# Kernel tuning notes

Hardware: AMD Instinct MI355X
Metric: run time of the kernel (lower is better)

The kernel has to match this reference:

```python
import jax, jax.numpy as jnp
import numpy as np

N_TREES = 512
DEPTH = 10
NODES_PER_TREE = 2 ** DEPTH - 1  # 1023, heap-indexed complete binary tree
N = N_TREES * NODES_PER_TREE     # 523776 nodes
X_SIZE = 128
H_SIZE = 128
NUM_CLASSES = 5
VOCAB = 32000


def _level_ids(l):
    """Global node ids for level l (root=0) and their child ids (None for leaves)."""
    start = 2 ** l - 1
    heap = start + np.arange(2 ** l)
    tree_off = np.arange(N_TREES)[:, None] * NODES_PER_TREE
    ids = (tree_off + heap[None, :]).reshape(-1)
    if l < DEPTH - 1:
        child_heap = np.stack([2 * heap + 1, 2 * heap + 2], axis=-1)  # [2^l, 2]
        child = (np.arange(N_TREES)[:, None, None] * NODES_PER_TREE
                 + child_heap[None]).reshape(-1, 2)
        return jnp.asarray(ids), jnp.asarray(child)
    return jnp.asarray(ids), None


def setup_inputs() -> dict:
    key = jax.random.key(0)
    ks = jax.random.split(key, 12)
    s = 0.05
    return {
        "wordid": jax.random.randint(ks[0], (N,), 0, VOCAB),
        "E":      jax.random.normal(ks[1], (VOCAB, X_SIZE), jnp.float32) * s,
        "W_iou":  jax.random.normal(ks[2], (3 * H_SIZE, X_SIZE), jnp.float32) * s,
        "b_iou":  jax.random.normal(ks[3], (3 * H_SIZE,), jnp.float32) * s,
        "U_iou":  jax.random.normal(ks[4], (3 * H_SIZE, H_SIZE), jnp.float32) * s,
        "b_Uiou": jax.random.normal(ks[5], (3 * H_SIZE,), jnp.float32) * s,
        "W_f":    jax.random.normal(ks[6], (H_SIZE, X_SIZE), jnp.float32) * s,
        "b_Wf":   jax.random.normal(ks[7], (H_SIZE,), jnp.float32) * s,
        "U_f":    jax.random.normal(ks[8], (H_SIZE, H_SIZE), jnp.float32) * s,
        "b_Uf":   jax.random.normal(ks[9], (H_SIZE,), jnp.float32) * s,
        "W_out":  jax.random.normal(ks[10], (NUM_CLASSES, H_SIZE), jnp.float32) * s,
        "b_out":  jax.random.normal(ks[11], (NUM_CLASSES,), jnp.float32) * s,
    }


def reference(wordid, E, W_iou, b_iou, U_iou, b_Uiou, W_f, b_Wf, U_f, b_Uf, W_out, b_out):
    mask = (wordid != -1)  # PAD_WORD mask; all-true for generated ids
    x = E[wordid * mask.astype(wordid.dtype)] * mask[:, None].astype(E.dtype)  # [N, X]

    h = jnp.zeros((N, H_SIZE), E.dtype)
    c = jnp.zeros((N, H_SIZE), E.dtype)

    # Topological traversal: leaves (deepest level) up to roots.
    for l in reversed(range(DEPTH)):
        ids, child = _level_ids(l)
        xl = x[ids]  # [M, X]
        if child is None:  # leaves: empty mailbox -> h_tild = c_tild = 0
            h_tild = jnp.zeros((ids.shape[0], H_SIZE), E.dtype)
            c_tild = h_tild
        else:
            hc = h[child]                               # mailbox h: [M, 2, H]
            cc = c[child]                               # mailbox c: [M, 2, H]
            h_tild = hc.sum(axis=1)                     # child-sum
            wx = xl @ W_f.T + b_Wf                      # [M, H]
            uh = hc @ U_f.T + b_Uf                      # [M, 2, H]
            f = jax.nn.sigmoid(wx[:, None, :] + uh)     # per-child forget gate
            c_tild = (f * cc).sum(axis=1)
        iou = xl @ W_iou.T + b_iou + h_tild @ U_iou.T + b_Uiou  # [M, 3H]
        i, o, u = jnp.split(iou, 3, axis=1)
        i, o, u = jax.nn.sigmoid(i), jax.nn.sigmoid(o), jnp.tanh(u)
        cl = i * u + c_tild
        hl = o * jnp.tanh(cl)
        h = h.at[ids].set(hl)
        c = c.at[ids].set(cl)

    # dropout is identity in eval / p=0.0
    logits = h @ W_out.T + b_out  # [N, num_classes]
    return logits
```

## Files before the change

kernel.cpp:

```cpp
#include <hip/hip_runtime.h>

#define H 128
#define TDEPTH 10
#define NPT 1023
#define NTREES 512

typedef unsigned short bf16_t;
typedef unsigned int u32;
typedef __attribute__((ext_vector_type(8))) short bf16x8;
typedef __attribute__((ext_vector_type(4))) float f32x4;

__device__ __forceinline__ float rcp_(float x) { return __builtin_amdgcn_rcpf(x); }
__device__ __forceinline__ float sig_(float x) { return rcp_(1.0f + __expf(-x)); }
__device__ __forceinline__ float th_(float x)  { return 1.0f - 2.0f * rcp_(__expf(2.0f * x) + 1.0f); }
__device__ __forceinline__ float b2f(u32 u) {
    union { float f; u32 u; } v; v.u = u << 16; return v.f;
}
__device__ __forceinline__ bf16_t f2b16(float f) {
    union { float f; u32 u; } v; v.f = f;
    return (bf16_t)((v.u + 0x7fffu + ((v.u >> 16) & 1u)) >> 16);
}
__device__ __forceinline__ bf16x8 ld8(const bf16_t* p) {
    return *reinterpret_cast<const bf16x8*>(p);
}
__device__ __forceinline__ bf16x8 ld8c(const char* p) {
    return *reinterpret_cast<const bf16x8*>(p);
}
__device__ __forceinline__ void gload16(const void* g, void* l) {
    __builtin_amdgcn_global_load_lds(
        (const __attribute__((address_space(1))) void*)g,
        (__attribute__((address_space(3))) void*)l, 16, 0, 0);
}
#define MFMA(a,b,c) __builtin_amdgcn_mfma_f32_16x16x32_bf16(a,b,c,0,0,0)

#define R_H  8192
#define R_C  24576
#define BUFSZ 40960

__global__ void pack_weights(const float* __restrict__ W_iou, const float* __restrict__ U_iou,
                             const float* __restrict__ W_f,   const float* __restrict__ U_f,
                             const float* __restrict__ W_out, bf16_t* __restrict__ Wb)
{
    int i = blockIdx.x * 256 + threadIdx.x;
    if (i < 131072) {
        int k    = i & 127;
        int p    = (i >> 7) & 7;
        int feat = i >> 10;
        float v;
        switch (p) {
            case 0: v = W_iou[(      feat) * H + k]; break;
            case 1: v = W_iou[(128 + feat) * H + k]; break;
            case 2: v = W_iou[(256 + feat) * H + k]; break;
            case 3: v = U_iou[(      feat) * H + k]; break;
            case 4: v = U_iou[(128 + feat) * H + k]; break;
            case 5: v = U_iou[(256 + feat) * H + k]; break;
            case 6: v = W_f  [feat * H + k]; break;
            default: v = U_f [feat * H + k]; break;
        }
        Wb[i] = f2b16(v);
    } else {
        int j = i - 131072;
        int cls = j >> 7, k = j & 127;
        Wb[i] = f2b16(cls < 5 ? W_out[cls * H + k] : 0.0f);
    }
}

__global__ void pack_E(const float* __restrict__ E, bf16_t* __restrict__ Eb)
{
    int i = blockIdx.x * 256 + threadIdx.x;
    Eb[i] = f2b16(E[i]);
}

__global__ __launch_bounds__(512, 4) void leaf_mfma(
    const int* __restrict__ wordid, const bf16_t* __restrict__ Eb,
    const bf16_t* __restrict__ Wb,
    const float* __restrict__ b_iou, const float* __restrict__ b_Uiou,
    bf16_t* __restrict__ h_cur, bf16_t* __restrict__ c_cur, int t0)
{
    const int level = TDEPTH - 1;
    __shared__ __align__(16) char x_s[64 * 256];

    const int tid = threadIdx.x;
    const int n0  = blockIdx.x * 64;

    for (int idx = tid; idx < 1024; idx += 512) {
        int q = idx & 15, m = idx >> 4;
        int g = n0 + m;
        int t = g >> level, i = g & ((1 << level) - 1);
        int wid = wordid[(t0 + t) * NPT + (1 << level) - 1 + i];
        *(uint4*)(x_s + m * 256 + ((q * 16) ^ ((m & 7) << 4))) =
            *(const uint4*)(Eb + (size_t)wid * H + q * 8);
    }
    __syncthreads();

    const int lane = tid & 63;
    const int w    = tid >> 6;
    const int l15  = lane & 15;
    const int kg   = lane >> 4;
    const int feat = w * 16 + l15;
    const bf16_t* wbase = Wb + (size_t)feat * 1024 + kg * 8;

    f32x4 z = {0.f, 0.f, 0.f, 0.f};
    f32x4 acc[3][4];
#pragma unroll
    for (int g = 0; g < 3; ++g)
#pragma unroll
        for (int m = 0; m < 4; ++m) acc[g][m] = z;

#pragma unroll
    for (int ks = 0; ks < 4; ++ks) {
        bf16x8 W0 = ld8(wbase + ks * 32 + 0 * 128);
        bf16x8 W1 = ld8(wbase + ks * 32 + 1 * 128);
        bf16x8 W2 = ld8(wbase + ks * 32 + 2 * 128);
        const int cb = (ks * 32 + kg * 8) * 2;
#pragma unroll
        for (int mt = 0; mt < 4; ++mt) {
            int row = mt * 16 + l15;
            bf16x8 xa = ld8c(x_s + row * 256 + (cb ^ ((row & 7) << 4)));
            acc[0][mt] = MFMA(xa, W0, acc[0][mt]);
            acc[1][mt] = MFMA(xa, W1, acc[1][mt]);
            acc[2][mt] = MFMA(xa, W2, acc[2][mt]);
        }
    }

    float bi = b_iou[      feat] + b_Uiou[      feat];
    float bo = b_iou[128 + feat] + b_Uiou[128 + feat];
    float bu = b_iou[256 + feat] + b_Uiou[256 + feat];
#pragma unroll
    for (int mt = 0; mt < 4; ++mt) {
#pragma unroll
        for (int r = 0; r < 4; ++r) {
            int g = n0 + mt * 16 + kg * 4 + r;
            float iv = sig_(acc[0][mt][r] + bi);
            float ov = sig_(acc[1][mt][r] + bo);
            float uv = th_ (acc[2][mt][r] + bu);
            float cl = iv * uv;
            float hl = ov * th_(cl);
            h_cur[(size_t)g * H + feat] = f2b16(hl);
            c_cur[(size_t)g * H + feat] = f2b16(cl);
        }
    }
}

__global__ __launch_bounds__(512, 2) void internal_mfma(
    const int* __restrict__ wordid, const bf16_t* __restrict__ Eb,
    const bf16_t* __restrict__ Wb,
    const float* __restrict__ b_iou, const float* __restrict__ b_Uiou,
    const float* __restrict__ b_Wf,  const float* __restrict__ b_Uf,
    const bf16_t* __restrict__ h_prev, const bf16_t* __restrict__ c_prev,
    bf16_t* __restrict__ h_cur, bf16_t* __restrict__ c_cur,
    const float* __restrict__ b_out, float* __restrict__ out,
    int level, int t0, int nt)
{
    extern __shared__ __align__(16) char lds_raw[];

    const int tid  = threadIdx.x;
    const int lane = tid & 63;
    const int w    = tid >> 6;
    const int l15  = lane & 15;
    const int kg   = lane >> 4;
    const int feat = w * 16 + l15;
    const int tilebase = blockIdx.x * nt;

    const float bi  = b_iou[      feat] + b_Uiou[      feat];
    const float bo  = b_iou[128 + feat] + b_Uiou[128 + feat];
    const float bu  = b_iou[256 + feat] + b_Uiou[256 + feat];
    const float bfv = b_Wf[feat] + b_Uf[feat];
    const bf16_t* wbase = Wb + (size_t)feat * 1024 + kg * 8;
    const f32x4 z = {0.f, 0.f, 0.f, 0.f};

    const int lrow = lane >> 4;
    const int colb = (lane & 15) * 16;

    auto issue = [&](int t, char* buf) {
        int n0 = (tilebase + t) * 32;
#pragma unroll
        for (int cc = 0; cc < 5; ++cc) {
            int ch = w + cc * 8;
            const char* src;
            if (ch < 8) {
                int row = ch * 4 + lrow;
                int g = n0 + row;
                int tt = g >> level, ii = g & ((1 << level) - 1);
                int wid = wordid[(t0 + tt) * NPT + (1 << level) - 1 + ii];
                src = (const char*)Eb + (size_t)wid * 256 + (colb ^ ((row & 7) << 4));
            } else if (ch < 24) {
                int row = (ch - 8) * 4 + lrow;
                src = (const char*)h_prev + ((size_t)(2 * n0) + row) * 256
                    + (colb ^ (((row >> 1) & 7) << 4));
            } else {
                int row = (ch - 24) * 4 + lrow;
                src = (const char*)c_prev + ((size_t)(2 * n0) + row) * 256
                    + (colb ^ ((row & 7) << 4));
            }
            gload16(src, buf + ch * 1024);
        }
    };

    issue(0, lds_raw);
    __syncthreads();

    for (int t = 0; t < nt; ++t) {
        char* buf = lds_raw + (t & 1) * BUFSZ;
        char* x_s = buf;
        char* h_s = buf + R_H;
        char* c_s = buf + R_C;
        const int n0 = (tilebase + t) * 32;

        f32x4 acc[6][2];
#pragma unroll
        for (int g = 0; g < 6; ++g)
#pragma unroll
            for (int m = 0; m < 2; ++m) acc[g][m] = z;

#pragma unroll
        for (int ks = 0; ks < 4; ++ks) {
            bf16x8 W0 = ld8(wbase + ks * 32 + 0 * 128);
            bf16x8 W1 = ld8(wbase + ks * 32 + 1 * 128);
            bf16x8 W2 = ld8(wbase + ks * 32 + 2 * 128);
            bf16x8 W3 = ld8(wbase + ks * 32 + 3 * 128);
            bf16x8 W4 = ld8(wbase + ks * 32 + 4 * 128);
            bf16x8 W5 = ld8(wbase + ks * 32 + 5 * 128);
            bf16x8 W6 = ld8(wbase + ks * 32 + 6 * 128);
            bf16x8 W7 = ld8(wbase + ks * 32 + 7 * 128);
            const int cb = (ks * 32 + kg * 8) * 2;
#pragma unroll
            for (int mt = 0; mt < 2; ++mt) {
                const int row = mt * 16 + l15;
                const int sw  = (row & 7) << 4;
                bf16x8 xa  = ld8c(x_s + row * 256 + (cb ^ sw));
                bf16x8 h0a = ld8c(h_s + (2 * row)     * 256 + (cb ^ sw));
                bf16x8 h1a = ld8c(h_s + (2 * row + 1) * 256 + (cb ^ sw));
                acc[0][mt] = MFMA(h1a, W3, MFMA(h0a, W3, MFMA(xa, W0, acc[0][mt])));
                acc[1][mt] = MFMA(h1a, W4, MFMA(h0a, W4, MFMA(xa, W1, acc[1][mt])));
                acc[2][mt] = MFMA(h1a, W5, MFMA(h0a, W5, MFMA(xa, W2, acc[2][mt])));
                acc[3][mt] = MFMA(xa,  W6, acc[3][mt]);
                acc[4][mt] = MFMA(h0a, W7, acc[4][mt]);
                acc[5][mt] = MFMA(h1a, W7, acc[5][mt]);
            }
        }

        if (w < 4) {
            const int pr = (w & 2) ? 1 : 0;
            const int mbase = (w & 1) * 16;
            const bf16_t* Wob = Wb + 131072;
            f32x4 lacc = z;
#pragma unroll
            for (int ks = 0; ks < 4; ++ks) {
                const int cb = (ks * 32 + kg * 8) * 2;
                int prow = mbase + l15;
                bf16x8 ha = ld8c(h_s + (size_t)(2 * prow + pr) * 256
                                 + (cb ^ ((prow & 7) << 4)));
                bf16x8 wo = ld8(Wob + (size_t)l15 * 128 + ks * 32 + kg * 8);
                lacc = MFMA(ha, wo, lacc);
            }
            if (l15 < 5) {
                float bo5 = b_out[l15];
                int lc = level + 1;
#pragma unroll
                for (int r = 0; r < 4; ++r) {
                    int m  = mbase + kg * 4 + r;
                    int gc = 2 * (n0 + m) + pr;
                    int tt = gc >> lc, ii = gc & ((1 << lc) - 1);
                    out[(size_t)((t0 + tt) * NPT + (1 << lc) - 1 + ii) * 5 + l15] = lacc[r] + bo5;
                }
            }
        }

        if (t + 1 < nt) issue(t + 1, lds_raw + ((t + 1) & 1) * BUFSZ);

#pragma unroll
        for (int mt = 0; mt < 2; ++mt) {
#pragma unroll
            for (int r = 0; r < 4; ++r) {
                int nb = mt * 16 + kg * 4 + r;
                int g  = n0 + nb;
                float iv = sig_(acc[0][mt][r] + bi);
                float ov = sig_(acc[1][mt][r] + bo);
                float uv = th_ (acc[2][mt][r] + bu);
                float fx = acc[3][mt][r];
                float f0 = sig_(fx + acc[4][mt][r] + bfv);
                float f1 = sig_(fx + acc[5][mt][r] + bfv);
                float c0 = b2f((u32)*(const bf16_t*)(c_s + (2 * nb) * 256
                              + ((feat * 2) ^ (((2 * nb) & 7) << 4))));
                float c1 = b2f((u32)*(const bf16_t*)(c_s + (2 * nb + 1) * 256
                              + ((feat * 2) ^ (((2 * nb + 1) & 7) << 4))));
                float cl = iv * uv + f0 * c0 + f1 * c1;
                float hl = ov * th_(cl);
                h_cur[(size_t)g * H + feat] = f2b16(hl);
                c_cur[(size_t)g * H + feat] = f2b16(cl);
            }
        }

        __syncthreads();
    }
}

__global__ void logits_root(
    const bf16_t* __restrict__ h0buf, const float* __restrict__ W_out,
    const float* __restrict__ b_out, float* __restrict__ out,
    int M, int t0)
{
    int wv     = (blockIdx.x * blockDim.x + threadIdx.x) >> 6;
    int lane   = threadIdx.x & 63;
    int nwaves = (gridDim.x * blockDim.x) >> 6;
    for (int g = wv; g < M; g += nwaves) {
        float h0 = b2f((u32)h0buf[(size_t)g * H + lane]);
        float h1 = b2f((u32)h0buf[(size_t)g * H + 64 + lane]);
#pragma unroll
        for (int c = 0; c < 5; ++c) {
            float p = h0 * W_out[c * H + lane] + h1 * W_out[c * H + 64 + lane];
#pragma unroll
            for (int off = 32; off >= 1; off >>= 1) p += __shfl_xor(p, off, 64);
            if (lane == 0) out[(size_t)(t0 + g) * NPT * 5 + c] = p + b_out[c];
        }
    }
}

extern "C" void kernel_launch(void* const* d_in, const int* in_sizes, int n_in,
                              void* d_out, int out_size, void* d_ws, size_t ws_size,
                              hipStream_t stream)
{
    (void)in_sizes; (void)n_in; (void)out_size;
    const int*   wordid = (const int*)  d_in[0];
    const float* E      = (const float*)d_in[1];
    const float* W_iou  = (const float*)d_in[2];
    const float* b_iou  = (const float*)d_in[3];
    const float* U_iou  = (const float*)d_in[4];
    const float* b_Uiou = (const float*)d_in[5];
    const float* W_f    = (const float*)d_in[6];
    const float* b_Wf   = (const float*)d_in[7];
    const float* U_f    = (const float*)d_in[8];
    const float* b_Uf   = (const float*)d_in[9];
    const float* W_out  = (const float*)d_in[10];
    const float* b_out  = (const float*)d_in[11];
    float* out = (float*)d_out;

    bf16_t* Wb = (bf16_t*)d_ws;
    bf16_t* Eb = Wb + 133120;
    bf16_t* dyn = Eb + (size_t)32000 * H;
    const size_t fixed_bytes = (133120 + (size_t)32000 * H) * 2;

    int C = 1;
    while (C < 16 && fixed_bytes + (size_t)(NTREES / C) * 393216u > ws_size) C <<= 1;
    const int T = NTREES / C;

    bf16_t* hA = dyn;
    bf16_t* cA = hA + (size_t)T * 512 * H;
    bf16_t* hB = cA + (size_t)T * 512 * H;
    bf16_t* cB = hB + (size_t)T * 256 * H;

    pack_weights<<<520, 256, 0, stream>>>(W_iou, U_iou, W_f, U_f, W_out, Wb);
    pack_E<<<16000, 256, 0, stream>>>(E, Eb);

    for (int chunk = 0; chunk < C; ++chunk) {
        int t0 = chunk * T;
        for (int l = TDEPTH - 1; l >= 0; --l) {
            int M = T << l;
            bf16_t* h_cur  = (l & 1) ? hA : hB;
            bf16_t* c_cur  = (l & 1) ? cA : cB;
            bf16_t* h_prev = (l & 1) ? hB : hA;
            bf16_t* c_prev = (l & 1) ? cB : cA;

            if (l == TDEPTH - 1) {
                leaf_mfma<<<M / 64, 512, 0, stream>>>(
                    wordid, Eb, Wb, b_iou, b_Uiou, h_cur, c_cur, t0);
            } else {
                int tiles  = M / 32;
                int blocks = tiles < 512 ? tiles : 512;
                int nt     = tiles / blocks;
                internal_mfma<<<blocks, 512, 2 * BUFSZ, stream>>>(
                    wordid, Eb, Wb, b_iou, b_Uiou, b_Wf, b_Uf,
                    h_prev, c_prev, h_cur, c_cur, b_out, out, l, t0, nt);
            }
        }
        int blocksR = (T / 4 < 4096) ? ((T + 3) / 4) : 4096;
        if (blocksR < 1) blocksR = 1;
        logits_root<<<blocksR, 256, 0, stream>>>(hB, W_out, b_out, out, T, t0);
    }
}
```

Baseline: 388.1 us.

## Hoist weight fragments into registers, issue prefetch earlier, halve internal grid

```diff
diff --git a/kernel.cpp b/kernel.cpp
--- a/kernel.cpp
+++ b/kernel.cpp
@@ -166,8 +166,20 @@
     const float bo  = b_iou[128 + feat] + b_Uiou[128 + feat];
     const float bu  = b_iou[256 + feat] + b_Uiou[256 + feat];
     const float bfv = b_Wf[feat] + b_Uf[feat];
+    const f32x4 z = {0.f, 0.f, 0.f, 0.f};
+
     const bf16_t* wbase = Wb + (size_t)feat * 1024 + kg * 8;
-    const f32x4 z = {0.f, 0.f, 0.f, 0.f};
+    const bf16_t* Wob   = Wb + 131072;
+    bf16x8 Wr[4][8];
+#pragma unroll
+    for (int ks = 0; ks < 4; ++ks)
+#pragma unroll
+        for (int p = 0; p < 8; ++p)
+            Wr[ks][p] = ld8(wbase + ks * 32 + p * 128);
+    bf16x8 Lr[4];
+#pragma unroll
+    for (int ks = 0; ks < 4; ++ks)
+        Lr[ks] = ld8(Wob + (size_t)l15 * 128 + ks * 32 + kg * 8);
 
     const int lrow = lane >> 4;
     const int colb = (lane & 15) * 16;
@@ -215,14 +227,6 @@
 
 #pragma unroll
         for (int ks = 0; ks < 4; ++ks) {
-            bf16x8 W0 = ld8(wbase + ks * 32 + 0 * 128);
-            bf16x8 W1 = ld8(wbase + ks * 32 + 1 * 128);
-            bf16x8 W2 = ld8(wbase + ks * 32 + 2 * 128);
-            bf16x8 W3 = ld8(wbase + ks * 32 + 3 * 128);
-            bf16x8 W4 = ld8(wbase + ks * 32 + 4 * 128);
-            bf16x8 W5 = ld8(wbase + ks * 32 + 5 * 128);
-            bf16x8 W6 = ld8(wbase + ks * 32 + 6 * 128);
-            bf16x8 W7 = ld8(wbase + ks * 32 + 7 * 128);
             const int cb = (ks * 32 + kg * 8) * 2;
 #pragma unroll
             for (int mt = 0; mt < 2; ++mt) {
@@ -231,19 +235,20 @@
                 bf16x8 xa  = ld8c(x_s + row * 256 + (cb ^ sw));
                 bf16x8 h0a = ld8c(h_s + (2 * row)     * 256 + (cb ^ sw));
                 bf16x8 h1a = ld8c(h_s + (2 * row + 1) * 256 + (cb ^ sw));
-                acc[0][mt] = MFMA(h1a, W3, MFMA(h0a, W3, MFMA(xa, W0, acc[0][mt])));
-                acc[1][mt] = MFMA(h1a, W4, MFMA(h0a, W4, MFMA(xa, W1, acc[1][mt])));
-                acc[2][mt] = MFMA(h1a, W5, MFMA(h0a, W5, MFMA(xa, W2, acc[2][mt])));
-                acc[3][mt] = MFMA(xa,  W6, acc[3][mt]);
-                acc[4][mt] = MFMA(h0a, W7, acc[4][mt]);
-                acc[5][mt] = MFMA(h1a, W7, acc[5][mt]);
-            }
-        }
+                acc[0][mt] = MFMA(h1a, Wr[ks][3], MFMA(h0a, Wr[ks][3], MFMA(xa, Wr[ks][0], acc[0][mt])));
+                acc[1][mt] = MFMA(h1a, Wr[ks][4], MFMA(h0a, Wr[ks][4], MFMA(xa, Wr[ks][1], acc[1][mt])));
+                acc[2][mt] = MFMA(h1a, Wr[ks][5], MFMA(h0a, Wr[ks][5], MFMA(xa, Wr[ks][2], acc[2][mt])));
+                acc[3][mt] = MFMA(xa,  Wr[ks][6], acc[3][mt]);
+                acc[4][mt] = MFMA(h0a, Wr[ks][7], acc[4][mt]);
+                acc[5][mt] = MFMA(h1a, Wr[ks][7], acc[5][mt]);
+            }
+        }
+
+        if (t + 1 < nt) issue(t + 1, lds_raw + ((t + 1) & 1) * BUFSZ);
 
         if (w < 4) {
             const int pr = (w & 2) ? 1 : 0;
             const int mbase = (w & 1) * 16;
-            const bf16_t* Wob = Wb + 131072;
             f32x4 lacc = z;
 #pragma unroll
             for (int ks = 0; ks < 4; ++ks) {
@@ -251,8 +256,7 @@
                 int prow = mbase + l15;
                 bf16x8 ha = ld8c(h_s + (size_t)(2 * prow + pr) * 256
                                  + (cb ^ ((prow & 7) << 4)));
-                bf16x8 wo = ld8(Wob + (size_t)l15 * 128 + ks * 32 + kg * 8);
-                lacc = MFMA(ha, wo, lacc);
+                lacc = MFMA(ha, Lr[ks], lacc);
             }
             if (l15 < 5) {
                 float bo5 = b_out[l15];
@@ -266,8 +270,6 @@
                 }
             }
         }
-
-        if (t + 1 < nt) issue(t + 1, lds_raw + ((t + 1) & 1) * BUFSZ);
 
 #pragma unroll
         for (int mt = 0; mt < 2; ++mt) {
@@ -367,7 +369,7 @@
                     wordid, Eb, Wb, b_iou, b_Uiou, h_cur, c_cur, t0);
             } else {
                 int tiles  = M / 32;
-                int blocks = tiles < 512 ? tiles : 512;
+                int blocks = tiles < 256 ? tiles : 256;
                 int nt     = tiles / blocks;
                 internal_mfma<<<blocks, 512, 2 * BUFSZ, stream>>>(
                     wordid, Eb, Wb, b_iou, b_Uiou, b_Wf, b_Uf,
```

Result: no change. 392.7 us (+1.2%).

## Halve internal tile to 16 nodes, prefetch word ids, issue next tile earlier

Applied to the files above, without the earlier changes.

```diff
diff --git a/kernel.cpp b/kernel.cpp
--- a/kernel.cpp
+++ b/kernel.cpp
@@ -33,9 +33,9 @@
 }
 #define MFMA(a,b,c) __builtin_amdgcn_mfma_f32_16x16x32_bf16(a,b,c,0,0,0)
 
-#define R_H  8192
-#define R_C  24576
-#define BUFSZ 40960
+#define R_H  4096
+#define R_C  12288
+#define BUFSZ 20480
 
 __global__ void pack_weights(const float* __restrict__ W_iou, const float* __restrict__ U_iou,
                              const float* __restrict__ W_f,   const float* __restrict__ U_f,
@@ -142,7 +142,7 @@
     }
 }
 
-__global__ __launch_bounds__(512, 2) void internal_mfma(
+__global__ __launch_bounds__(512, 4) void internal_mfma(
     const int* __restrict__ wordid, const bf16_t* __restrict__ Eb,
     const bf16_t* __restrict__ Wb,
     const float* __restrict__ b_iou, const float* __restrict__ b_Uiou,
@@ -166,38 +166,48 @@
     const float bo  = b_iou[128 + feat] + b_Uiou[128 + feat];
     const float bu  = b_iou[256 + feat] + b_Uiou[256 + feat];
     const float bfv = b_Wf[feat] + b_Uf[feat];
+    const f32x4 z = {0.f, 0.f, 0.f, 0.f};
+
     const bf16_t* wbase = Wb + (size_t)feat * 1024 + kg * 8;
-    const f32x4 z = {0.f, 0.f, 0.f, 0.f};
+    const bf16_t* Wob   = Wb + 131072;
 
     const int lrow = lane >> 4;
     const int colb = (lane & 15) * 16;
 
-    auto issue = [&](int t, char* buf) {
-        int n0 = (tilebase + t) * 32;
-#pragma unroll
-        for (int cc = 0; cc < 5; ++cc) {
+    auto loadwid = [&](int n0x) -> int {
+        int row = w * 4 + lrow;
+        int g = n0x + row;
+        int tt = g >> level, ii = g & ((1 << level) - 1);
+        return wordid[(t0 + tt) * NPT + (1 << level) - 1 + ii];
+    };
+
+    auto issue = [&](int n0x, int widv, char* buf) {
+#pragma unroll
+        for (int cc = 0; cc < 3; ++cc) {
             int ch = w + cc * 8;
-            const char* src;
-            if (ch < 8) {
-                int row = ch * 4 + lrow;
-                int g = n0 + row;
-                int tt = g >> level, ii = g & ((1 << level) - 1);
-                int wid = wordid[(t0 + tt) * NPT + (1 << level) - 1 + ii];
-                src = (const char*)Eb + (size_t)wid * 256 + (colb ^ ((row & 7) << 4));
-            } else if (ch < 24) {
-                int row = (ch - 8) * 4 + lrow;
-                src = (const char*)h_prev + ((size_t)(2 * n0) + row) * 256
-                    + (colb ^ (((row >> 1) & 7) << 4));
-            } else {
-                int row = (ch - 24) * 4 + lrow;
-                src = (const char*)c_prev + ((size_t)(2 * n0) + row) * 256
-                    + (colb ^ ((row & 7) << 4));
+            if (ch < 20) {
+                const char* src;
+                if (ch < 4) {
+                    int row = ch * 4 + lrow;
+                    src = (const char*)Eb + (size_t)widv * 256 + (colb ^ ((row & 7) << 4));
+                } else if (ch < 12) {
+                    int j = (ch - 4) * 4 + lrow;
+                    src = (const char*)h_prev + ((size_t)(2 * n0x) + j) * 256
+                        + (colb ^ (((j >> 1) & 7) << 4));
+                } else {
+                    int j = (ch - 12) * 4 + lrow;
+                    src = (const char*)c_prev + ((size_t)(2 * n0x) + j) * 256
+                        + (colb ^ ((j & 7) << 4));
+                }
+                gload16(src, buf + ch * 1024);
             }
-            gload16(src, buf + ch * 1024);
         }
     };
 
-    issue(0, lds_raw);
+    int widcur = 0;
+    if (w < 4) widcur = loadwid(tilebase * 16);
+    issue(tilebase * 16, widcur, lds_raw);
+    if (nt > 1 && w < 4) widcur = loadwid((tilebase + 1) * 16);
     __syncthreads();
 
     for (int t = 0; t < nt; ++t) {
@@ -205,13 +215,16 @@
         char* x_s = buf;
         char* h_s = buf + R_H;
         char* c_s = buf + R_C;
-        const int n0 = (tilebase + t) * 32;
-
-        f32x4 acc[6][2];
-#pragma unroll
-        for (int g = 0; g < 6; ++g)
-#pragma unroll
-            for (int m = 0; m < 2; ++m) acc[g][m] = z;
+        const int n0 = (tilebase + t) * 16;
+
+        if (t + 1 < nt)
+            issue((tilebase + t + 1) * 16, widcur, lds_raw + ((t + 1) & 1) * BUFSZ);
+        int widnext = widcur;
+        if (t + 2 < nt && w < 4) widnext = loadwid((tilebase + t + 2) * 16);
+
+        f32x4 acc[6];
+#pragma unroll
+        for (int g = 0; g < 6; ++g) acc[g] = z;
 
 #pragma unroll
         for (int ks = 0; ks < 4; ++ks) {
@@ -224,33 +237,26 @@
             bf16x8 W6 = ld8(wbase + ks * 32 + 6 * 128);
             bf16x8 W7 = ld8(wbase + ks * 32 + 7 * 128);
             const int cb = (ks * 32 + kg * 8) * 2;
-#pragma unroll
-            for (int mt = 0; mt < 2; ++mt) {
-                const int row = mt * 16 + l15;
-                const int sw  = (row & 7) << 4;
-                bf16x8 xa  = ld8c(x_s + row * 256 + (cb ^ sw));
-                bf16x8 h0a = ld8c(h_s + (2 * row)     * 256 + (cb ^ sw));
-                bf16x8 h1a = ld8c(h_s + (2 * row + 1) * 256 + (cb ^ sw));
-                acc[0][mt] = MFMA(h1a, W3, MFMA(h0a, W3, MFMA(xa, W0, acc[0][mt])));
-                acc[1][mt] = MFMA(h1a, W4, MFMA(h0a, W4, MFMA(xa, W1, acc[1][mt])));
-                acc[2][mt] = MFMA(h1a, W5, MFMA(h0a, W5, MFMA(xa, W2, acc[2][mt])));
-                acc[3][mt] = MFMA(xa,  W6, acc[3][mt]);
-                acc[4][mt] = MFMA(h0a, W7, acc[4][mt]);
-                acc[5][mt] = MFMA(h1a, W7, acc[5][mt]);
-            }
-        }
-
-        if (w < 4) {
-            const int pr = (w & 2) ? 1 : 0;
-            const int mbase = (w & 1) * 16;
-            const bf16_t* Wob = Wb + 131072;
+            const int sw = (l15 & 7) << 4;
+            bf16x8 xa  = ld8c(x_s + l15 * 256 + (cb ^ sw));
+            bf16x8 h0a = ld8c(h_s + (2 * l15)     * 256 + (cb ^ sw));
+            bf16x8 h1a = ld8c(h_s + (2 * l15 + 1) * 256 + (cb ^ sw));
+            acc[0] = MFMA(h1a, W3, MFMA(h0a, W3, MFMA(xa, W0, acc[0])));
+            acc[1] = MFMA(h1a, W4, MFMA(h0a, W4, MFMA(xa, W1, acc[1])));
+            acc[2] = MFMA(h1a, W5, MFMA(h0a, W5, MFMA(xa, W2, acc[2])));
+            acc[3] = MFMA(xa,  W6, acc[3]);
+            acc[4] = MFMA(h0a, W7, acc[4]);
+            acc[5] = MFMA(h1a, W7, acc[5]);
+        }
+
+        if (w < 2) {
+            const int pr = w;
             f32x4 lacc = z;
 #pragma unroll
             for (int ks = 0; ks < 4; ++ks) {
                 const int cb = (ks * 32 + kg * 8) * 2;
-                int prow = mbase + l15;
-                bf16x8 ha = ld8c(h_s + (size_t)(2 * prow + pr) * 256
-                                 + (cb ^ ((prow & 7) << 4)));
+                bf16x8 ha = ld8c(h_s + (size_t)(2 * l15 + pr) * 256
+                                 + (cb ^ ((l15 & 7) << 4)));
                 bf16x8 wo = ld8(Wob + (size_t)l15 * 128 + ks * 32 + kg * 8);
                 lacc = MFMA(ha, wo, lacc);
             }
@@ -259,7 +265,7 @@
                 int lc = level + 1;
 #pragma unroll
                 for (int r = 0; r < 4; ++r) {
-                    int m  = mbase + kg * 4 + r;
+                    int m  = kg * 4 + r;
                     int gc = 2 * (n0 + m) + pr;
                     int tt = gc >> lc, ii = gc & ((1 << lc) - 1);
                     out[(size_t)((t0 + tt) * NPT + (1 << lc) - 1 + ii) * 5 + l15] = lacc[r] + bo5;
@@ -267,31 +273,27 @@
             }
         }
 
-        if (t + 1 < nt) issue(t + 1, lds_raw + ((t + 1) & 1) * BUFSZ);
-
-#pragma unroll
-        for (int mt = 0; mt < 2; ++mt) {
-#pragma unroll
-            for (int r = 0; r < 4; ++r) {
-                int nb = mt * 16 + kg * 4 + r;
-                int g  = n0 + nb;
-                float iv = sig_(acc[0][mt][r] + bi);
-                float ov = sig_(acc[1][mt][r] + bo);
-                float uv = th_ (acc[2][mt][r] + bu);
-                float fx = acc[3][mt][r];
-                float f0 = sig_(fx + acc[4][mt][r] + bfv);
-                float f1 = sig_(fx + acc[5][mt][r] + bfv);
-                float c0 = b2f((u32)*(const bf16_t*)(c_s + (2 * nb) * 256
-                              + ((feat * 2) ^ (((2 * nb) & 7) << 4))));
-                float c1 = b2f((u32)*(const bf16_t*)(c_s + (2 * nb + 1) * 256
-                              + ((feat * 2) ^ (((2 * nb + 1) & 7) << 4))));
-                float cl = iv * uv + f0 * c0 + f1 * c1;
-                float hl = ov * th_(cl);
-                h_cur[(size_t)g * H + feat] = f2b16(hl);
-                c_cur[(size_t)g * H + feat] = f2b16(cl);
-            }
-        }
-
+#pragma unroll
+        for (int r = 0; r < 4; ++r) {
+            int nb = kg * 4 + r;
+            int g  = n0 + nb;
+            float iv = sig_(acc[0][r] + bi);
+            float ov = sig_(acc[1][r] + bo);
+            float uv = th_ (acc[2][r] + bu);
+            float fx = acc[3][r];
+            float f0 = sig_(fx + acc[4][r] + bfv);
+            float f1 = sig_(fx + acc[5][r] + bfv);
+            float c0 = b2f((u32)*(const bf16_t*)(c_s + (2 * nb) * 256
+                          + ((feat * 2) ^ (((2 * nb) & 7) << 4))));
+            float c1 = b2f((u32)*(const bf16_t*)(c_s + (2 * nb + 1) * 256
+                          + ((feat * 2) ^ (((2 * nb + 1) & 7) << 4))));
+            float cl = iv * uv + f0 * c0 + f1 * c1;
+            float hl = ov * th_(cl);
+            h_cur[(size_t)g * H + feat] = f2b16(hl);
+            c_cur[(size_t)g * H + feat] = f2b16(cl);
+        }
+
+        widcur = widnext;
         __syncthreads();
     }
 }
@@ -366,7 +368,7 @@
                 leaf_mfma<<<M / 64, 512, 0, stream>>>(
                     wordid, Eb, Wb, b_iou, b_Uiou, h_cur, c_cur, t0);
             } else {
-                int tiles  = M / 32;
+                int tiles  = M / 16;
                 int blocks = tiles < 512 ? tiles : 512;
                 int nt     = tiles / blocks;
                 internal_mfma<<<blocks, 512, 2 * BUFSZ, stream>>>(
```

Measured after the change: 708.0 us. 82.5% more time.

## Fuse leaf level and its parent level into one kernel via LDS

Applied to the files above, without the earlier changes.

```diff
diff --git a/kernel.cpp b/kernel.cpp
--- a/kernel.cpp
+++ b/kernel.cpp
@@ -36,6 +36,11 @@
 #define R_H  8192
 #define R_C  24576
 #define BUFSZ 40960
+
+#define FX_SZ   24576
+#define F_H     49152
+#define F_C     65536
+#define F_LDSSZ 81920
 
 __global__ void pack_weights(const float* __restrict__ W_iou, const float* __restrict__ U_iou,
                              const float* __restrict__ W_f,   const float* __restrict__ U_f,
@@ -71,74 +76,204 @@
     Eb[i] = f2b16(E[i]);
 }
 
-__global__ __launch_bounds__(512, 4) void leaf_mfma(
+__global__ __launch_bounds__(512, 2) void leaf8_fused(
     const int* __restrict__ wordid, const bf16_t* __restrict__ Eb,
     const bf16_t* __restrict__ Wb,
     const float* __restrict__ b_iou, const float* __restrict__ b_Uiou,
-    bf16_t* __restrict__ h_cur, bf16_t* __restrict__ c_cur, int t0)
+    const float* __restrict__ b_Wf,  const float* __restrict__ b_Uf,
+    bf16_t* __restrict__ h_cur, bf16_t* __restrict__ c_cur,
+    const float* __restrict__ b_out, float* __restrict__ out,
+    int t0, int nt)
 {
-    const int level = TDEPTH - 1;
-    __shared__ __align__(16) char x_s[64 * 256];
-
-    const int tid = threadIdx.x;
-    const int n0  = blockIdx.x * 64;
-
-    for (int idx = tid; idx < 1024; idx += 512) {
-        int q = idx & 15, m = idx >> 4;
-        int g = n0 + m;
-        int t = g >> level, i = g & ((1 << level) - 1);
-        int wid = wordid[(t0 + t) * NPT + (1 << level) - 1 + i];
-        *(uint4*)(x_s + m * 256 + ((q * 16) ^ ((m & 7) << 4))) =
-            *(const uint4*)(Eb + (size_t)wid * H + q * 8);
-    }
-    __syncthreads();
-
+    extern __shared__ __align__(16) char lds_raw[];
+
+    const int tid  = threadIdx.x;
     const int lane = tid & 63;
     const int w    = tid >> 6;
     const int l15  = lane & 15;
     const int kg   = lane >> 4;
     const int feat = w * 16 + l15;
+    const int tilebase = blockIdx.x * nt;
+
+    const float bi  = b_iou[      feat] + b_Uiou[      feat];
+    const float bo  = b_iou[128 + feat] + b_Uiou[128 + feat];
+    const float bu  = b_iou[256 + feat] + b_Uiou[256 + feat];
+    const float bfv = b_Wf[feat] + b_Uf[feat];
+    const f32x4 z = {0.f, 0.f, 0.f, 0.f};
+
     const bf16_t* wbase = Wb + (size_t)feat * 1024 + kg * 8;
-
-    f32x4 z = {0.f, 0.f, 0.f, 0.f};
-    f32x4 acc[3][4];
-#pragma unroll
-    for (int g = 0; g < 3; ++g)
-#pragma unroll
-        for (int m = 0; m < 4; ++m) acc[g][m] = z;
-
-#pragma unroll
-    for (int ks = 0; ks < 4; ++ks) {
-        bf16x8 W0 = ld8(wbase + ks * 32 + 0 * 128);
-        bf16x8 W1 = ld8(wbase + ks * 32 + 1 * 128);
-        bf16x8 W2 = ld8(wbase + ks * 32 + 2 * 128);
-        const int cb = (ks * 32 + kg * 8) * 2;
+    const bf16_t* Wob   = Wb + 131072;
+
+    const int lrow = lane >> 4;
+    const int colb = (lane & 15) * 16;
+
+    struct Wids { int a, b, c; };
+    auto loadwid = [&](int t) -> Wids {
+        Wids r;
+        int tb64 = (tilebase + t) * 64, tb32 = (tilebase + t) * 32;
+        {   int gl = tb64 + w * 4 + lrow;
+            int tt = gl >> 9, ii = gl & 511;
+            r.a = wordid[(t0 + tt) * NPT + 511 + ii]; }
+        {   int gl = tb64 + 32 + w * 4 + lrow;
+            int tt = gl >> 9, ii = gl & 511;
+            r.b = wordid[(t0 + tt) * NPT + 511 + ii]; }
+        {   int gp = tb32 + w * 4 + lrow;
+            int tt = gp >> 8, ii = gp & 255;
+            r.c = wordid[(t0 + tt) * NPT + 255 + ii]; }
+        return r;
+    };
+
+    auto issue = [&](const Wids& wd, char* xbuf) {
+        {   int row = w * 4 + lrow;
+            gload16((const char*)Eb + (size_t)wd.a * 256 + (colb ^ ((row & 7) << 4)),
+                    xbuf + w * 1024); }
+        {   int row = 32 + w * 4 + lrow;
+            gload16((const char*)Eb + (size_t)wd.b * 256 + (colb ^ ((row & 7) << 4)),
+                    xbuf + (w + 8) * 1024); }
+        {   int row = w * 4 + lrow;
+            gload16((const char*)Eb + (size_t)wd.c * 256 + (colb ^ ((row & 7) << 4)),
+                    xbuf + (w + 16) * 1024); }
+    };
+
+    Wids wcur = loadwid(0);
+    issue(wcur, lds_raw);
+    if (nt > 1) wcur = loadwid(1);
+    __syncthreads();
+
+    char* h_s = lds_raw + F_H;
+    char* c_s = lds_raw + F_C;
+
+    for (int t = 0; t < nt; ++t) {
+        char* xbuf  = lds_raw + (t & 1) * FX_SZ;
+        char* xleaf = xbuf;
+        char* xpar  = xbuf + 16384;
+        const int n0 = (tilebase + t) * 32;
+
+        f32x4 lac[3][4];
+#pragma unroll
+        for (int g = 0; g < 3; ++g)
+#pragma unroll
+            for (int m = 0; m < 4; ++m) lac[g][m] = z;
+
+#pragma unroll
+        for (int ks = 0; ks < 4; ++ks) {
+            bf16x8 W0 = ld8(wbase + ks * 32 + 0 * 128);
+            bf16x8 W1 = ld8(wbase + ks * 32 + 1 * 128);
+            bf16x8 W2 = ld8(wbase + ks * 32 + 2 * 128);
+            const int cb = (ks * 32 + kg * 8) * 2;
+#pragma unroll
+            for (int mt = 0; mt < 4; ++mt) {
+                int row = mt * 16 + l15;
+                bf16x8 xa = ld8c(xleaf + row * 256 + (cb ^ ((row & 7) << 4)));
+                lac[0][mt] = MFMA(xa, W0, lac[0][mt]);
+                lac[1][mt] = MFMA(xa, W1, lac[1][mt]);
+                lac[2][mt] = MFMA(xa, W2, lac[2][mt]);
+            }
+        }
+
+        if (t + 1 < nt) {
+            issue(wcur, lds_raw + ((t + 1) & 1) * FX_SZ);
+            if (t + 2 < nt) wcur = loadwid(t + 2);
+        }
+
 #pragma unroll
         for (int mt = 0; mt < 4; ++mt) {
-            int row = mt * 16 + l15;
-            bf16x8 xa = ld8c(x_s + row * 256 + (cb ^ ((row & 7) << 4)));
-            acc[0][mt] = MFMA(xa, W0, acc[0][mt]);
-            acc[1][mt] = MFMA(xa, W1, acc[1][mt]);
-            acc[2][mt] = MFMA(xa, W2, acc[2][mt]);
-        }
-    }
-
-    float bi = b_iou[      feat] + b_Uiou[      feat];
-    float bo = b_iou[128 + feat] + b_Uiou[128 + feat];
-    float bu = b_iou[256 + feat] + b_Uiou[256 + feat];
-#pragma unroll
-    for (int mt = 0; mt < 4; ++mt) {
-#pragma unroll
-        for (int r = 0; r < 4; ++r) {
-            int g = n0 + mt * 16 + kg * 4 + r;
-            float iv = sig_(acc[0][mt][r] + bi);
-            float ov = sig_(acc[1][mt][r] + bo);
-            float uv = th_ (acc[2][mt][r] + bu);
-            float cl = iv * uv;
-            float hl = ov * th_(cl);
-            h_cur[(size_t)g * H + feat] = f2b16(hl);
-            c_cur[(size_t)g * H + feat] = f2b16(cl);
-        }
+#pragma unroll
+            for (int r = 0; r < 4; ++r) {
+                int j = mt * 16 + kg * 4 + r;
+                float iv = sig_(lac[0][mt][r] + bi);
+                float ov = sig_(lac[1][mt][r] + bo);
+                float uv = th_ (lac[2][mt][r] + bu);
+                float cl = iv * uv;
+                float hl = ov * th_(cl);
+                *(bf16_t*)(h_s + j * 256 + ((feat * 2) ^ (((j >> 1) & 7) << 4))) = f2b16(hl);
+                *(bf16_t*)(c_s + j * 256 + ((feat * 2) ^ ((j & 7) << 4)))        = f2b16(cl);
+            }
+        }
+        __syncthreads();
+
+        f32x4 acc[6][2];
+#pragma unroll
+        for (int g = 0; g < 6; ++g)
+#pragma unroll
+            for (int m = 0; m < 2; ++m) acc[g][m] = z;
+
+#pragma unroll
+        for (int ks = 0; ks < 4; ++ks) {
+            bf16x8 W0 = ld8(wbase + ks * 32 + 0 * 128);
+            bf16x8 W1 = ld8(wbase + ks * 32 + 1 * 128);
+            bf16x8 W2 = ld8(wbase + ks * 32 + 2 * 128);
+            bf16x8 W3 = ld8(wbase + ks * 32 + 3 * 128);
+            bf16x8 W4 = ld8(wbase + ks * 32 + 4 * 128);
+            bf16x8 W5 = ld8(wbase + ks * 32 + 5 * 128);
+            bf16x8 W6 = ld8(wbase + ks * 32 + 6 * 128);
+            bf16x8 W7 = ld8(wbase + ks * 32 + 7 * 128);
+            const int cb = (ks * 32 + kg * 8) * 2;
+#pragma unroll
+            for (int mt = 0; mt < 2; ++mt) {
+                const int row = mt * 16 + l15;
+                const int sw  = (row & 7) << 4;
+                bf16x8 xa  = ld8c(xpar + row * 256 + (cb ^ sw));
+                bf16x8 h0a = ld8c(h_s + (2 * row)     * 256 + (cb ^ sw));
+                bf16x8 h1a = ld8c(h_s + (2 * row + 1) * 256 + (cb ^ sw));
+                acc[0][mt] = MFMA(h1a, W3, MFMA(h0a, W3, MFMA(xa, W0, acc[0][mt])));
+                acc[1][mt] = MFMA(h1a, W4, MFMA(h0a, W4, MFMA(xa, W1, acc[1][mt])));
+                acc[2][mt] = MFMA(h1a, W5, MFMA(h0a, W5, MFMA(xa, W2, acc[2][mt])));
+                acc[3][mt] = MFMA(xa,  W6, acc[3][mt]);
+                acc[4][mt] = MFMA(h0a, W7, acc[4][mt]);
+                acc[5][mt] = MFMA(h1a, W7, acc[5][mt]);
+            }
+        }
+
+        if (w < 4) {
+            const int pr = (w & 2) ? 1 : 0;
+            const int mbase = (w & 1) * 16;
+            f32x4 lacc = z;
+#pragma unroll
+            for (int ks = 0; ks < 4; ++ks) {
+                const int cb = (ks * 32 + kg * 8) * 2;
+                int prow = mbase + l15;
+                bf16x8 ha = ld8c(h_s + (size_t)(2 * prow + pr) * 256
+                                 + (cb ^ ((prow & 7) << 4)));
+                bf16x8 wo = ld8(Wob + (size_t)l15 * 128 + ks * 32 + kg * 8);
+                lacc = MFMA(ha, wo, lacc);
+            }
+            if (l15 < 5) {
+                float bo5 = b_out[l15];
+#pragma unroll
+                for (int r = 0; r < 4; ++r) {
+                    int m  = mbase + kg * 4 + r;
+                    int gc = 2 * (n0 + m) + pr;
+                    int tt = gc >> 9, ii = gc & 511;
+                    out[(size_t)((t0 + tt) * NPT + 511 + ii) * 5 + l15] = lacc[r] + bo5;
+                }
+            }
+        }
+
+#pragma unroll
+        for (int mt = 0; mt < 2; ++mt) {
+#pragma unroll
+            for (int r = 0; r < 4; ++r) {
+                int nb = mt * 16 + kg * 4 + r;
+                int g  = n0 + nb;
+                float iv = sig_(acc[0][mt][r] + bi);
+                float ov = sig_(acc[1][mt][r] + bo);
+                float uv = th_ (acc[2][mt][r] + bu);
+                float fx = acc[3][mt][r];
+                float f0 = sig_(fx + acc[4][mt][r] + bfv);
+                float f1 = sig_(fx + acc[5][mt][r] + bfv);
+                float c0 = b2f((u32)*(const bf16_t*)(c_s + (2 * nb) * 256
+                              + ((feat * 2) ^ (((2 * nb) & 7) << 4))));
+                float c1 = b2f((u32)*(const bf16_t*)(c_s + (2 * nb + 1) * 256
+                              + ((feat * 2) ^ (((2 * nb + 1) & 7) << 4))));
+                float cl = iv * uv + f0 * c0 + f1 * c1;
+                float hl = ov * th_(cl);
+                h_cur[(size_t)g * H + feat] = f2b16(hl);
+                c_cur[(size_t)g * H + feat] = f2b16(cl);
+            }
+        }
+
+        __syncthreads();
     }
 }
 
@@ -166,8 +301,10 @@
     const float bo  = b_iou[128 + feat] + b_Uiou[128 + feat];
     const float bu  = b_iou[256 + feat] + b_Uiou[256 + feat];
     const float bfv = b_Wf[feat] + b_Uf[feat];
+    const f32x4 z = {0.f, 0.f, 0.f, 0.f};
+
     const bf16_t* wbase = Wb + (size_t)feat * 1024 + kg * 8;
-    const f32x4 z = {0.f, 0.f, 0.f, 0.f};
+    const bf16_t* Wob   = Wb + 131072;
 
     const int lrow = lane >> 4;
     const int colb = (lane & 15) * 16;
@@ -215,6 +352,7 @@
 
 #pragma unroll
         for (int ks = 0; ks < 4; ++ks) {
+            const int cb = (ks * 32 + kg * 8) * 2;
             bf16x8 W0 = ld8(wbase + ks * 32 + 0 * 128);
             bf16x8 W1 = ld8(wbase + ks * 32 + 1 * 128);
             bf16x8 W2 = ld8(wbase + ks * 32 + 2 * 128);
@@ -223,7 +361,6 @@
             bf16x8 W5 = ld8(wbase + ks * 32 + 5 * 128);
             bf16x8 W6 = ld8(wbase + ks * 32 + 6 * 128);
             bf16x8 W7 = ld8(wbase + ks * 32 + 7 * 128);
-            const int cb = (ks * 32 + kg * 8) * 2;
 #pragma unroll
             for (int mt = 0; mt < 2; ++mt) {
                 const int row = mt * 16 + l15;
@@ -240,10 +377,11 @@
             }
         }
 
+        if (t + 1 < nt) issue(t + 1, lds_raw + ((t + 1) & 1) * BUFSZ);
+
         if (w < 4) {
             const int pr = (w & 2) ? 1 : 0;
             const int mbase = (w & 1) * 16;
-            const bf16_t* Wob = Wb + 131072;
             f32x4 lacc = z;
 #pragma unroll
             for (int ks = 0; ks < 4; ++ks) {
@@ -266,8 +404,6 @@
                 }
             }
         }
-
-        if (t + 1 < nt) issue(t + 1, lds_raw + ((t + 1) & 1) * BUFSZ);
 
 #pragma unroll
         for (int mt = 0; mt < 2; ++mt) {
@@ -342,12 +478,12 @@
     const size_t fixed_bytes = (133120 + (size_t)32000 * H) * 2;
 
     int C = 1;
-    while (C < 16 && fixed_bytes + (size_t)(NTREES / C) * 393216u > ws_size) C <<= 1;
+    while (C < 16 && fixed_bytes + (size_t)(NTREES / C) * 262144u > ws_size) C <<= 1;
     const int T = NTREES / C;
 
     bf16_t* hA = dyn;
-    bf16_t* cA = hA + (size_t)T * 512 * H;
-    bf16_t* hB = cA + (size_t)T * 512 * H;
+    bf16_t* cA = hA + (size_t)T * 256 * H;
+    bf16_t* hB = cA + (size_t)T * 256 * H;
     bf16_t* cB = hB + (size_t)T * 256 * H;
 
     pack_weights<<<520, 256, 0, stream>>>(W_iou, U_iou, W_f, U_f, W_out, Wb);
@@ -355,24 +491,30 @@
 
     for (int chunk = 0; chunk < C; ++chunk) {
         int t0 = chunk * T;
-        for (int l = TDEPTH - 1; l >= 0; --l) {
+
+        {
+            int tiles  = (T << 8) / 32;
+            int blocks = tiles < 256 ? tiles : 256;
+            int nt     = tiles / blocks;
+            leaf8_fused<<<blocks, 512, F_LDSSZ, stream>>>(
+                wordid, Eb, Wb, b_iou, b_Uiou, b_Wf, b_Uf,
+                hB, cB, b_out, out, t0, nt);
+        }
+
+        for (int l = TDEPTH - 3; l >= 0; --l) {
             int M = T << l;
             bf16_t* h_cur  = (l & 1) ? hA : hB;
             bf16_t* c_cur  = (l & 1) ? cA : cB;
             bf16_t* h_prev = (l & 1) ? hB : hA;
             bf16_t* c_prev = (l & 1) ? cB : cA;
 
-            if (l == TDEPTH - 1) {
-                leaf_mfma<<<M / 64, 512, 0, stream>>>(
-                    wordid, Eb, Wb, b_iou, b_Uiou, h_cur, c_cur, t0);
-            } else {
-                int tiles  = M / 32;
-                int blocks = tiles < 512 ? tiles : 512;
-                int nt     = tiles / blocks;
-                internal_mfma<<<blocks, 512, 2 * BUFSZ, stream>>>(
-                    wordid, Eb, Wb, b_iou, b_Uiou, b_Wf, b_Uf,
-                    h_prev, c_prev, h_cur, c_cur, b_out, out, l, t0, nt);
-            }
+            int tiles  = M / 32;
+            int blocks = tiles < 256 ? tiles : 256;
+            if (blocks < 1) blocks = 1;
+            int nt     = tiles / blocks;
+            internal_mfma<<<blocks, 512, 2 * BUFSZ, stream>>>(
+                wordid, Eb, Wb, b_iou, b_Uiou, b_Wf, b_Uf,
+                h_prev, c_prev, h_cur, c_cur, b_out, out, l, t0, nt);
         }
         int blocksR = (T / 4 < 4096) ? ((T + 3) / 4) : 4096;
         if (blocksR < 1) blocksR = 1;
```

Measured after the change: 348.1 us. 1.11x faster.
